# Optimization experiments

Hardware: AMD Instinct MI355X
Metric: run time of the kernel (lower is better)

## Reference

```python
import jax, jax.numpy as jnp
import numpy as np

BITS_W = 2  # WAGE default weight bitwidth


def _scale(bits):
    return 2.0 ** (bits - 1)


def quantize_w(x):
    """WAGE Quantize.W: clip to [-1+delta, 1-delta], round to grid of step delta,
    with straight-through estimator for gradients."""
    s = _scale(BITS_W)
    delta = 1.0 / s
    xc = jnp.clip(x, -1.0 + delta, 1.0 - delta)
    y = jnp.round(xc * s) / s
    # straight-through: forward uses y, gradient flows as identity to x
    return x + jax.lax.stop_gradient(y - x)


def setup_inputs() -> dict:
    key = jax.random.key(0)
    k1, k2 = jax.random.split(key)
    B, D_IN, C_OUT = 16384, 1024, 1024
    inputs = jax.random.normal(k1, (B, D_IN), dtype=jnp.float32)
    # learned kernel per build(): shape [d_in, c_out]
    kernel = jax.random.normal(k2, (D_IN, C_OUT), dtype=jnp.float32) * 0.5
    return {"inputs": inputs, "kernel": kernel}


def reference(inputs, kernel):
    # quantize weights every forward pass, then dense matmul
    return jnp.matmul(inputs, quantize_w(kernel))
```

## Files before the change

### kernel.cpp

```cpp
#include <hip/hip_runtime.h>

typedef unsigned short u16;
typedef unsigned int u32;

typedef __bf16 bf16x8 __attribute__((ext_vector_type(8)));
typedef float floatx4 __attribute__((ext_vector_type(4)));


__device__ __forceinline__ u32 f2bf(float f) {
    u32 u = __builtin_bit_cast(u32, f);
    return (u + 0x7fffu + ((u >> 16) & 1u)) >> 16;
}

__device__ __forceinline__ float quant_w(float x) {
    float xc = fminf(fmaxf(x, -0.5f), 0.5f);
    return rintf(xc * 2.0f) * 0.5f;
}

__device__ __forceinline__ void gload_lds16(const u16* g, u16* l) {
    __builtin_amdgcn_global_load_lds(
        (const __attribute__((address_space(1))) void*)g,
        (__attribute__((address_space(3))) void*)l,
        16, 0, 0);
}


__global__ __launch_bounds__(256) void cast_a_kernel(const float4* __restrict__ in,
                                                     uint4* __restrict__ out) {
    int t = blockIdx.x * 256 + threadIdx.x;
    float4 a = in[2 * t];
    float4 b = in[2 * t + 1];
    uint4 o;
    o.x = f2bf(a.x) | (f2bf(a.y) << 16);
    o.y = f2bf(a.z) | (f2bf(a.w) << 16);
    o.z = f2bf(b.x) | (f2bf(b.y) << 16);
    o.w = f2bf(b.z) | (f2bf(b.w) << 16);
    out[t] = o;
}


__global__ __launch_bounds__(256) void quant_transpose_kernel(const float* __restrict__ W,
                                                              u16* __restrict__ Bt) {
    __shared__ u16 tile[32][33];
    const int KN = 1024;
    int tx = threadIdx.x;
    int ty = threadIdx.y;
    int k0 = blockIdx.y * 32;
    int n0 = blockIdx.x * 32;
#pragma unroll
    for (int i = 0; i < 4; i++) {
        int kl = ty + i * 8;
        float x = W[(k0 + kl) * KN + n0 + tx];
        tile[kl][tx] = (u16)f2bf(quant_w(x));
    }
    __syncthreads();
#pragma unroll
    for (int i = 0; i < 4; i++) {
        int nl = ty + i * 8;
        Bt[(n0 + nl) * KN + k0 + tx] = tile[tx][nl];
    }
}


__global__ __launch_bounds__(256) void gemm_bt_kernel(const u16* __restrict__ A,
                                                      const u16* __restrict__ Bt,
                                                      float* __restrict__ C) {
    const int K = 1024;
    const int N = 1024;

    __shared__ alignas(16) u16 As[128 * 64];
    __shared__ alignas(16) u16 Bs[128 * 64];

    const int tid = threadIdx.x;
    const int mbase = blockIdx.x * 128;
    const int nbase = blockIdx.y * 128;
    const int lane = tid & 63;
    const int wv = tid >> 6;
    const int wm = (wv & 1) * 64;
    const int wn = (wv >> 1) * 64;
    const int frow = lane & 15;
    const int fkc = lane >> 4;
    const int rsw = frow & 7;

    floatx4 acc[4][4] = {};

    const int srow = tid >> 3;
    const int g8 = (tid & 7) ^ (srow & 7);
    const u16* Aga[4];
    const u16* Bga[4];
#pragma unroll
    for (int q = 0; q < 4; q++) {
        Aga[q] = &A[(size_t)(mbase + q * 32 + srow) * K + g8 * 8];
        Bga[q] = &Bt[(size_t)(nbase + q * 32 + srow) * K + g8 * 8];
    }

    for (int kt = 0; kt < K; kt += 64) {
        __syncthreads();
#pragma unroll
        for (int q = 0; q < 4; q++) {
            gload_lds16(Aga[q] + kt, &As[(q * 256 + tid) * 8]);
            gload_lds16(Bga[q] + kt, &Bs[(q * 256 + tid) * 8]);
        }
        __syncthreads();

#pragma unroll
        for (int s = 0; s < 2; s++) {
            bf16x8 af[4], bf[4];
#pragma unroll
            for (int i = 0; i < 4; i++)
                af[i] = *(const bf16x8*)&As[(wm + i * 16 + frow) * 64 +
                                            (((s * 4 + fkc) ^ rsw) * 8)];
#pragma unroll
            for (int j = 0; j < 4; j++)
                bf[j] = *(const bf16x8*)&Bs[(wn + j * 16 + frow) * 64 +
                                            (((s * 4 + fkc) ^ rsw) * 8)];
#pragma unroll
            for (int i = 0; i < 4; i++)
#pragma unroll
                for (int j = 0; j < 4; j++)
                    acc[i][j] = __builtin_amdgcn_mfma_f32_16x16x32_bf16(
                        af[i], bf[j], acc[i][j], 0, 0, 0);
        }
    }

    const int crow = (lane >> 4) * 4;
    const int ccol = lane & 15;
#pragma unroll
    for (int i = 0; i < 4; i++) {
#pragma unroll
        for (int j = 0; j < 4; j++) {
            float* cp = &C[(size_t)(mbase + wm + i * 16 + crow) * N + nbase + wn + j * 16 + ccol];
#pragma unroll
            for (int r = 0; r < 4; r++) cp[r * N] = acc[i][j][r];
        }
    }
}


extern "C" void kernel_launch(void* const* d_in, const int* in_sizes, int n_in,
                              void* d_out, int out_size, void* d_ws, size_t ws_size,
                              hipStream_t stream) {
    const float* A = (const float*)d_in[0];
    const float* W = (const float*)d_in[1];
    float* C = (float*)d_out;

    u16* Abf = (u16*)d_ws;
    u16* Btq = (u16*)((char*)d_ws + (size_t)33554432);

    cast_a_kernel<<<8192, 256, 0, stream>>>((const float4*)A, (uint4*)Abf);
    quant_transpose_kernel<<<dim3(32, 32), dim3(32, 8), 0, stream>>>(W, Btq);
    gemm_bt_kernel<<<dim3(128, 8), 256, 0, stream>>>(Abf, Btq, C);
}
```

Before: 151.8 us.

## Double-buffer GEMM LDS tiles with BK=32 and merge prep kernels into one launch

The GEMM main loop now uses two LDS buffers with a K-tile of 32 and issues the next tile's global-to-LDS loads before computing the current one, so each iteration needs one barrier instead of two. The XOR swizzle is reworked for the 32-wide rows. The activation cast and the weight quantize-transpose are merged into a single launch, removing one kernel launch. The risk is that a halved K-tile doubles the loop iterations and barriers, and since it relies on global_load_lds ordering under a single barrier it may expose load latency or sync hazards.

```diff
diff --git a/kernel.cpp b/kernel.cpp
--- a/kernel.cpp
+++ b/kernel.cpp
@@ -25,39 +25,42 @@
 }
 
 
-__global__ __launch_bounds__(256) void cast_a_kernel(const float4* __restrict__ in,
-                                                     uint4* __restrict__ out) {
-    int t = blockIdx.x * 256 + threadIdx.x;
-    float4 a = in[2 * t];
-    float4 b = in[2 * t + 1];
-    uint4 o;
-    o.x = f2bf(a.x) | (f2bf(a.y) << 16);
-    o.y = f2bf(a.z) | (f2bf(a.w) << 16);
-    o.z = f2bf(b.x) | (f2bf(b.y) << 16);
-    o.w = f2bf(b.z) | (f2bf(b.w) << 16);
-    out[t] = o;
-}
-
-
-__global__ __launch_bounds__(256) void quant_transpose_kernel(const float* __restrict__ W,
-                                                              u16* __restrict__ Bt) {
-    __shared__ u16 tile[32][33];
-    const int KN = 1024;
-    int tx = threadIdx.x;
-    int ty = threadIdx.y;
-    int k0 = blockIdx.y * 32;
-    int n0 = blockIdx.x * 32;
+__global__ __launch_bounds__(256) void prep_kernel(const float4* __restrict__ Af,
+                                                   uint4* __restrict__ Abf,
+                                                   const float* __restrict__ W,
+                                                   u16* __restrict__ Bt) {
+    const int bid = blockIdx.x;
+    const int tid = threadIdx.x;
+    if (bid < 8192) {
+        int t = bid * 256 + tid;
+        float4 a = Af[2 * t];
+        float4 b = Af[2 * t + 1];
+        uint4 o;
+        o.x = f2bf(a.x) | (f2bf(a.y) << 16);
+        o.y = f2bf(a.z) | (f2bf(a.w) << 16);
+        o.z = f2bf(b.x) | (f2bf(b.y) << 16);
+        o.w = f2bf(b.z) | (f2bf(b.w) << 16);
+        Abf[t] = o;
+    } else {
+        __shared__ u16 tile[32][33];
+        const int KN = 1024;
+        int b = bid - 8192;
+        int n0 = (b & 31) * 32;
+        int k0 = (b >> 5) * 32;
+        int tx = tid & 31;
+        int ty = tid >> 5;
 #pragma unroll
-    for (int i = 0; i < 4; i++) {
-        int kl = ty + i * 8;
-        float x = W[(k0 + kl) * KN + n0 + tx];
-        tile[kl][tx] = (u16)f2bf(quant_w(x));
-    }
-    __syncthreads();
+        for (int i = 0; i < 4; i++) {
+            int kl = ty + i * 8;
+            float x = W[(k0 + kl) * KN + n0 + tx];
+            tile[kl][tx] = (u16)f2bf(quant_w(x));
+        }
+        __syncthreads();
 #pragma unroll
-    for (int i = 0; i < 4; i++) {
-        int nl = ty + i * 8;
-        Bt[(n0 + nl) * KN + k0 + tx] = tile[tx][nl];
+        for (int i = 0; i < 4; i++) {
+            int nl = ty + i * 8;
+            Bt[(n0 + nl) * KN + k0 + tx] = tile[tx][nl];
+        }
     }
 }
 
@@ -68,8 +71,8 @@
     const int K = 1024;
     const int N = 1024;
 
-    __shared__ alignas(16) u16 As[128 * 64];
-    __shared__ alignas(16) u16 Bs[128 * 64];
+    __shared__ alignas(16) u16 As[2][128 * 32];
+    __shared__ alignas(16) u16 Bs[2][128 * 32];
 
     const int tid = threadIdx.x;
     const int mbase = blockIdx.x * 128;
@@ -80,47 +83,49 @@
     const int wn = (wv >> 1) * 64;
     const int frow = lane & 15;
     const int fkc = lane >> 4;
-    const int rsw = frow & 7;
+    const int koff = ((fkc ^ ((frow >> 1) & 3)) * 8);
+
+    const int c0 = tid, c1 = tid + 256;
+    const int r0 = c0 >> 2, r1 = c1 >> 2;
+    const int g0 = (c0 & 3) ^ ((r0 >> 1) & 3);
+    const int g1 = (c1 & 3) ^ ((r1 >> 1) & 3);
+    const u16* Ag0 = &A[(size_t)(mbase + r0) * K + g0 * 8];
+    const u16* Ag1 = &A[(size_t)(mbase + r1) * K + g1 * 8];
+    const u16* Bg0 = &Bt[(size_t)(nbase + r0) * K + g0 * 8];
+    const u16* Bg1 = &Bt[(size_t)(nbase + r1) * K + g1 * 8];
 
     floatx4 acc[4][4] = {};
 
-    const int srow = tid >> 3;
-    const int g8 = (tid & 7) ^ (srow & 7);
-    const u16* Aga[4];
-    const u16* Bga[4];
+    gload_lds16(Ag0, &As[0][c0 * 8]);
+    gload_lds16(Ag1, &As[0][c1 * 8]);
+    gload_lds16(Bg0, &Bs[0][c0 * 8]);
+    gload_lds16(Bg1, &Bs[0][c1 * 8]);
+
+    for (int it = 0; it < 32; ++it) {
+        __syncthreads();
+        const int cur = it & 1;
+        const int nxt = cur ^ 1;
+        if (it + 1 < 32) {
+            const int kt = (it + 1) * 32;
+            gload_lds16(Ag0 + kt, &As[nxt][c0 * 8]);
+            gload_lds16(Ag1 + kt, &As[nxt][c1 * 8]);
+            gload_lds16(Bg0 + kt, &Bs[nxt][c0 * 8]);
+            gload_lds16(Bg1 + kt, &Bs[nxt][c1 * 8]);
+        }
+
+        bf16x8 af[4], bf[4];
 #pragma unroll
-    for (int q = 0; q < 4; q++) {
-        Aga[q] = &A[(size_t)(mbase + q * 32 + srow) * K + g8 * 8];
-        Bga[q] = &Bt[(size_t)(nbase + q * 32 + srow) * K + g8 * 8];
-    }
-
-    for (int kt = 0; kt < K; kt += 64) {
-        __syncthreads();
+        for (int i = 0; i < 4; i++)
+            af[i] = *(const bf16x8*)&As[cur][(wm + i * 16 + frow) * 32 + koff];
 #pragma unroll
-        for (int q = 0; q < 4; q++) {
-            gload_lds16(Aga[q] + kt, &As[(q * 256 + tid) * 8]);
-            gload_lds16(Bga[q] + kt, &Bs[(q * 256 + tid) * 8]);
-        }
-        __syncthreads();
-
+        for (int j = 0; j < 4; j++)
+            bf[j] = *(const bf16x8*)&Bs[cur][(wn + j * 16 + frow) * 32 + koff];
 #pragma unroll
-        for (int s = 0; s < 2; s++) {
-            bf16x8 af[4], bf[4];
-#pragma unroll
-            for (int i = 0; i < 4; i++)
-                af[i] = *(const bf16x8*)&As[(wm + i * 16 + frow) * 64 +
-                                            (((s * 4 + fkc) ^ rsw) * 8)];
+        for (int i = 0; i < 4; i++)
 #pragma unroll
             for (int j = 0; j < 4; j++)
-                bf[j] = *(const bf16x8*)&Bs[(wn + j * 16 + frow) * 64 +
-                                            (((s * 4 + fkc) ^ rsw) * 8)];
-#pragma unroll
-            for (int i = 0; i < 4; i++)
-#pragma unroll
-                for (int j = 0; j < 4; j++)
-                    acc[i][j] = __builtin_amdgcn_mfma_f32_16x16x32_bf16(
-                        af[i], bf[j], acc[i][j], 0, 0, 0);
-        }
+                acc[i][j] = __builtin_amdgcn_mfma_f32_16x16x32_bf16(
+                    af[i], bf[j], acc[i][j], 0, 0, 0);
     }
 
     const int crow = (lane >> 4) * 4;
@@ -147,7 +152,6 @@
     u16* Abf = (u16*)d_ws;
     u16* Btq = (u16*)((char*)d_ws + (size_t)33554432);
 
-    cast_a_kernel<<<8192, 256, 0, stream>>>((const float4*)A, (uint4*)Abf);
-    quant_transpose_kernel<<<dim3(32, 32), dim3(32, 8), 0, stream>>>(W, Btq);
+    prep_kernel<<<8192 + 1024, 256, 0, stream>>>((const float4*)A, (uint4*)Abf, W, Btq);
     gemm_bt_kernel<<<dim3(128, 8), 256, 0, stream>>>(Abf, Btq, C);
 }
```

Measured after the change: 154.9 us. 2.0% more time.

## Merge prep kernels into one launch and enlarge GEMM tile to 256x128

Applied to the files above, without the earlier changes.

Fuses the activation bf16 cast and the weight quantize-transpose into a single launch whose block index selects the work, removing one kernel launch and the gap between them. The GEMM switches to 512-thread blocks covering a 256x128 output tile with 8 waves, which raises B-tile reuse per block and halves the block count. The larger tile increases LDS use per block (48KB) and may reduce occupancy, and 512 blocks on the device may leave some CUs underfilled.

```diff
diff --git a/kernel.cpp b/kernel.cpp
--- a/kernel.cpp
+++ b/kernel.cpp
@@ -25,82 +25,87 @@
 }
 
 
-__global__ __launch_bounds__(256) void cast_a_kernel(const float4* __restrict__ in,
-                                                     uint4* __restrict__ out) {
-    int t = blockIdx.x * 256 + threadIdx.x;
-    float4 a = in[2 * t];
-    float4 b = in[2 * t + 1];
-    uint4 o;
-    o.x = f2bf(a.x) | (f2bf(a.y) << 16);
-    o.y = f2bf(a.z) | (f2bf(a.w) << 16);
-    o.z = f2bf(b.x) | (f2bf(b.y) << 16);
-    o.w = f2bf(b.z) | (f2bf(b.w) << 16);
-    out[t] = o;
-}
-
-
-__global__ __launch_bounds__(256) void quant_transpose_kernel(const float* __restrict__ W,
-                                                              u16* __restrict__ Bt) {
-    __shared__ u16 tile[32][33];
-    const int KN = 1024;
-    int tx = threadIdx.x;
-    int ty = threadIdx.y;
-    int k0 = blockIdx.y * 32;
-    int n0 = blockIdx.x * 32;
+__global__ __launch_bounds__(256) void prep_kernel(const float4* __restrict__ Af,
+                                                   uint4* __restrict__ Abf,
+                                                   const float* __restrict__ W,
+                                                   u16* __restrict__ Bt) {
+    const int bid = blockIdx.x;
+    const int tid = threadIdx.x;
+    if (bid < 8192) {
+        int t = bid * 256 + tid;
+        float4 a = Af[2 * t];
+        float4 b = Af[2 * t + 1];
+        uint4 o;
+        o.x = f2bf(a.x) | (f2bf(a.y) << 16);
+        o.y = f2bf(a.z) | (f2bf(a.w) << 16);
+        o.z = f2bf(b.x) | (f2bf(b.y) << 16);
+        o.w = f2bf(b.z) | (f2bf(b.w) << 16);
+        Abf[t] = o;
+    } else {
+        __shared__ u16 tile[32][33];
+        const int KN = 1024;
+        int b = bid - 8192;
+        int n0 = (b & 31) * 32;
+        int k0 = (b >> 5) * 32;
+        int tx = tid & 31;
+        int ty = tid >> 5;
 #pragma unroll
-    for (int i = 0; i < 4; i++) {
-        int kl = ty + i * 8;
-        float x = W[(k0 + kl) * KN + n0 + tx];
-        tile[kl][tx] = (u16)f2bf(quant_w(x));
-    }
-    __syncthreads();
+        for (int i = 0; i < 4; i++) {
+            int kl = ty + i * 8;
+            float x = W[(k0 + kl) * KN + n0 + tx];
+            tile[kl][tx] = (u16)f2bf(quant_w(x));
+        }
+        __syncthreads();
 #pragma unroll
-    for (int i = 0; i < 4; i++) {
-        int nl = ty + i * 8;
-        Bt[(n0 + nl) * KN + k0 + tx] = tile[tx][nl];
+        for (int i = 0; i < 4; i++) {
+            int nl = ty + i * 8;
+            Bt[(n0 + nl) * KN + k0 + tx] = tile[tx][nl];
+        }
     }
 }
 
 
-__global__ __launch_bounds__(256) void gemm_bt_kernel(const u16* __restrict__ A,
+__global__ __launch_bounds__(512) void gemm_bt_kernel(const u16* __restrict__ A,
                                                       const u16* __restrict__ Bt,
                                                       float* __restrict__ C) {
     const int K = 1024;
     const int N = 1024;
 
-    __shared__ alignas(16) u16 As[128 * 64];
+    __shared__ alignas(16) u16 As[256 * 64];
     __shared__ alignas(16) u16 Bs[128 * 64];
 
     const int tid = threadIdx.x;
-    const int mbase = blockIdx.x * 128;
+    const int mbase = blockIdx.x * 256;
     const int nbase = blockIdx.y * 128;
     const int lane = tid & 63;
     const int wv = tid >> 6;
-    const int wm = (wv & 1) * 64;
-    const int wn = (wv >> 1) * 64;
+    const int wm = (wv & 3) * 64;
+    const int wn = (wv >> 2) * 64;
     const int frow = lane & 15;
     const int fkc = lane >> 4;
     const int rsw = frow & 7;
 
-    floatx4 acc[4][4] = {};
-
     const int srow = tid >> 3;
     const int g8 = (tid & 7) ^ (srow & 7);
     const u16* Aga[4];
-    const u16* Bga[4];
+    const u16* Bga[2];
 #pragma unroll
-    for (int q = 0; q < 4; q++) {
-        Aga[q] = &A[(size_t)(mbase + q * 32 + srow) * K + g8 * 8];
-        Bga[q] = &Bt[(size_t)(nbase + q * 32 + srow) * K + g8 * 8];
-    }
+    for (int q = 0; q < 4; q++)
+        Aga[q] = &A[(size_t)(mbase + q * 64 + srow) * K + g8 * 8];
+#pragma unroll
+    for (int q = 0; q < 2; q++)
+        Bga[q] = &Bt[(size_t)(nbase + q * 64 + srow) * K + g8 * 8];
+
+    floatx4 acc[4][4] = {};
 
     for (int kt = 0; kt < K; kt += 64) {
         __syncthreads();
 #pragma unroll
-        for (int q = 0; q < 4; q++) {
-            gload_lds16(Aga[q] + kt, &As[(q * 256 + tid) * 8]);
-            gload_lds16(Bga[q] + kt, &Bs[(q * 256 + tid) * 8]);
-        }
+        for (int q = 0; q < 4; q++)
+            gload_lds16(Aga[q] + kt, &As[(q * 512 + tid) * 8]);
+#pragma unroll
+        for (int q = 0; q < 2; q++)
+            gload_lds16(Bga[q] + kt, &Bs[(q * 512 + tid) * 8]);
         __syncthreads();
 
 #pragma unroll
@@ -147,7 +152,6 @@
     u16* Abf = (u16*)d_ws;
     u16* Btq = (u16*)((char*)d_ws + (size_t)33554432);
 
-    cast_a_kernel<<<8192, 256, 0, stream>>>((const float4*)A, (uint4*)Abf);
-    quant_transpose_kernel<<<dim3(32, 32), dim3(32, 8), 0, stream>>>(W, Btq);
-    gemm_bt_kernel<<<dim3(128, 8), 256, 0, stream>>>(Abf, Btq, C);
+    prep_kernel<<<8192 + 1024, 256, 0, stream>>>((const float4*)A, (uint4*)Abf, W, Btq);
+    gemm_bt_kernel<<<dim3(64, 8), 512, 0, stream>>>(Abf, Btq, C);
 }
```

Measured after the change: 158.6 us. 1.04x slower.

## Fuse fp32-to-bf16 activation cast into GEMM with register prefetch

Applied to the files above, without the earlier changes.

Removes the separate cast kernel and its bf16 workspace round trip. The GEMM now loads fp32 rows of A into registers one k-tile ahead, converts them to bf16 with a cheaper round-half-up pack, and writes them into swizzled LDS. B still goes through direct global-to-LDS loads. Each of the 8 N-blocks now rereads fp32 A, which is twice the bytes of bf16. The faster rounding also differs slightly from round-to-nearest-even.

```diff
diff --git a/kernel.cpp b/kernel.cpp
--- a/kernel.cpp
+++ b/kernel.cpp
@@ -7,9 +7,15 @@
 typedef float floatx4 __attribute__((ext_vector_type(4)));
 
 
-__device__ __forceinline__ u32 f2bf(float f) {
+__device__ __forceinline__ u32 f2bf_rne(float f) {
     u32 u = __builtin_bit_cast(u32, f);
     return (u + 0x7fffu + ((u >> 16) & 1u)) >> 16;
+}
+
+__device__ __forceinline__ u32 pack_bf2(float lo, float hi) {
+    u32 a = __builtin_bit_cast(u32, lo) + 0x8000u;
+    u32 b = __builtin_bit_cast(u32, hi) + 0x8000u;
+    return (a >> 16) | (b & 0xffff0000u);
 }
 
 __device__ __forceinline__ float quant_w(float x) {
@@ -25,33 +31,21 @@
 }
 
 
-__global__ __launch_bounds__(256) void cast_a_kernel(const float4* __restrict__ in,
-                                                     uint4* __restrict__ out) {
-    int t = blockIdx.x * 256 + threadIdx.x;
-    float4 a = in[2 * t];
-    float4 b = in[2 * t + 1];
-    uint4 o;
-    o.x = f2bf(a.x) | (f2bf(a.y) << 16);
-    o.y = f2bf(a.z) | (f2bf(a.w) << 16);
-    o.z = f2bf(b.x) | (f2bf(b.y) << 16);
-    o.w = f2bf(b.z) | (f2bf(b.w) << 16);
-    out[t] = o;
-}
-
-
-__global__ __launch_bounds__(256) void quant_transpose_kernel(const float* __restrict__ W,
-                                                              u16* __restrict__ Bt) {
+__global__ __launch_bounds__(256) void quantW_kernel(const float* __restrict__ W,
+                                                     u16* __restrict__ Bt) {
     __shared__ u16 tile[32][33];
     const int KN = 1024;
-    int tx = threadIdx.x;
-    int ty = threadIdx.y;
-    int k0 = blockIdx.y * 32;
-    int n0 = blockIdx.x * 32;
+    const int tid = threadIdx.x;
+    int b = blockIdx.x;
+    int n0 = (b & 31) * 32;
+    int k0 = (b >> 5) * 32;
+    int tx = tid & 31;
+    int ty = tid >> 5;
 #pragma unroll
     for (int i = 0; i < 4; i++) {
         int kl = ty + i * 8;
         float x = W[(k0 + kl) * KN + n0 + tx];
-        tile[kl][tx] = (u16)f2bf(quant_w(x));
+        tile[kl][tx] = (u16)f2bf_rne(quant_w(x));
     }
     __syncthreads();
 #pragma unroll
@@ -62,9 +56,9 @@
 }
 
 
-__global__ __launch_bounds__(256) void gemm_bt_kernel(const u16* __restrict__ A,
-                                                      const u16* __restrict__ Bt,
-                                                      float* __restrict__ C) {
+__global__ __launch_bounds__(256) void gemm_fused_kernel(const float* __restrict__ A,
+                                                         const u16* __restrict__ Bt,
+                                                         float* __restrict__ C) {
     const int K = 1024;
     const int N = 1024;
 
@@ -82,26 +76,47 @@
     const int fkc = lane >> 4;
     const int rsw = frow & 7;
 
-    floatx4 acc[4][4] = {};
+    const int ar = tid >> 1;
+    const int ah = tid & 1;
+    const float* Aga = &A[(size_t)(mbase + ar) * K + ah * 32];
+    u16* AsRow = &As[ar * 64];
+    const int asw = ar & 7;
 
     const int srow = tid >> 3;
     const int g8 = (tid & 7) ^ (srow & 7);
-    const u16* Aga[4];
     const u16* Bga[4];
 #pragma unroll
-    for (int q = 0; q < 4; q++) {
-        Aga[q] = &A[(size_t)(mbase + q * 32 + srow) * K + g8 * 8];
+    for (int q = 0; q < 4; q++)
         Bga[q] = &Bt[(size_t)(nbase + q * 32 + srow) * K + g8 * 8];
-    }
 
+    floatx4 acc[4][4] = {};
+
+    floatx4 pf[8];
+#pragma unroll
+    for (int j = 0; j < 8; j++) pf[j] = *(const floatx4*)&Aga[j * 4];
+
+#pragma unroll 1
     for (int kt = 0; kt < K; kt += 64) {
         __syncthreads();
 #pragma unroll
-        for (int q = 0; q < 4; q++) {
-            gload_lds16(Aga[q] + kt, &As[(q * 256 + tid) * 8]);
+        for (int q = 0; q < 4; q++)
             gload_lds16(Bga[q] + kt, &Bs[(q * 256 + tid) * 8]);
+#pragma unroll
+        for (int j2 = 0; j2 < 4; j2++) {
+            uint4 o;
+            o.x = pack_bf2(pf[2 * j2].x, pf[2 * j2].y);
+            o.y = pack_bf2(pf[2 * j2].z, pf[2 * j2].w);
+            o.z = pack_bf2(pf[2 * j2 + 1].x, pf[2 * j2 + 1].y);
+            o.w = pack_bf2(pf[2 * j2 + 1].z, pf[2 * j2 + 1].w);
+            int p = (ah * 4 + j2) ^ asw;
+            *(uint4*)&AsRow[p * 8] = o;
         }
         __syncthreads();
+
+        if (kt + 64 < K) {
+#pragma unroll
+            for (int j = 0; j < 8; j++) pf[j] = *(const floatx4*)&Aga[kt + 64 + j * 4];
+        }
 
 #pragma unroll
         for (int s = 0; s < 2; s++) {
@@ -144,10 +159,8 @@
     const float* W = (const float*)d_in[1];
     float* C = (float*)d_out;
 
-    u16* Abf = (u16*)d_ws;
-    u16* Btq = (u16*)((char*)d_ws + (size_t)33554432);
+    u16* Btq = (u16*)d_ws;
 
-    cast_a_kernel<<<8192, 256, 0, stream>>>((const float4*)A, (uint4*)Abf);
-    quant_transpose_kernel<<<dim3(32, 32), dim3(32, 8), 0, stream>>>(W, Btq);
-    gemm_bt_kernel<<<dim3(128, 8), 256, 0, stream>>>(Abf, Btq, C);
+    quantW_kernel<<<1024, 256, 0, stream>>>(W, Btq);
+    gemm_fused_kernel<<<dim3(128, 8), 256, 0, stream>>>(A, Btq, C);
 }
```

Result: slower. 184.3 us (+21.4%).
